# Kernel tuning notes

Hardware: AMD Instinct MI355X
Metric: run time of the kernel (lower is better)

The kernel has to match this reference:

```python
import jax, jax.numpy as jnp
import numpy as np

B, S, D, H, DK, DV, SEG = 2, 4096, 1024, 8, 128, 128, 512
NSEG = S // SEG


def setup_inputs() -> dict:
    key = jax.random.key(0)
    k0, k1, k2, k3, k4, k5 = jax.random.split(key, 6)
    return {
        "x": jax.random.normal(k0, (B, S, D), jnp.float32),
        "Wk": jax.random.normal(k1, (H, D, DK), jnp.float32) / np.float32(np.sqrt(D)),
        "Wv": jax.random.normal(k2, (H, D, DV), jnp.float32) / np.float32(np.sqrt(D)),
        "Wq": jax.random.normal(k3, (H, D, DK), jnp.float32) / np.float32(np.sqrt(D)),
        "Wout": jax.random.normal(k4, (H * DV, D), jnp.float32) / np.float32(np.sqrt(H * DV)),
        "betas": jax.random.normal(k5, (1, H, 1, DV), jnp.float32),
    }


def reference(x, Wk, Wv, Wq, Wout, betas):
    # Per-head projections: (B,H,S,dk/dv)
    k_full = jnp.einsum('bsd,hdk->bhsk', x, Wk)
    v_full = jnp.einsum('bsd,hdk->bhsk', x, Wv)
    q_full = jnp.einsum('bsd,hdk->bhsk', x, Wq)

    def to_segs(t):  # (B,H,S,E) -> (NSEG,B,H,SEG,E)
        return t.reshape(B, H, NSEG, SEG, t.shape[-1]).transpose(2, 0, 1, 3, 4)

    segs = (to_segs(k_full), to_segs(v_full), to_segs(q_full))

    mem0 = jnp.zeros((B, H, DK, DV), x.dtype)           # compressive memory
    z0 = jnp.full((B, H, DK, 1), 1.0 / DK, x.dtype)     # normalizer
    causal_mask = jnp.tril(jnp.ones((SEG, SEG), bool))
    gate = jax.nn.sigmoid(betas)                        # (1,H,1,DV)
    scale = jnp.asarray(1.0 / np.sqrt(DK), x.dtype)

    def step(carry, seg):
        mem, z = carry
        k, v, q = seg                                   # (B,H,SEG,dk/dv)
        sigma_q = jax.nn.elu(q) + 1.0
        # segment-local causal softmax attention
        scores = jnp.einsum('bhik,bhjk->bhij', q, k) * scale
        scores = jnp.where(causal_mask, scores, -jnp.inf)
        att_dot = jax.nn.softmax(scores, axis=-1) @ v
        # linear-attention read from memory
        att_mem = (sigma_q @ mem) / (sigma_q @ z)
        # delta-rule memory update
        sigma_k = jax.nn.elu(k) + 1.0
        mem = mem + jnp.einsum('bhsk,bhsv->bhkv', sigma_k, v - (sigma_k @ mem) / (sigma_k @ z))
        z = z + jnp.sum(sigma_k, axis=-2, keepdims=True).swapaxes(-1, -2)
        # gated mix of memory and local attention
        att = gate * att_mem + (1.0 - gate) * att_dot   # (B,H,SEG,DV)
        att = att.transpose(0, 2, 1, 3).reshape(B, SEG, H * DV)
        return (mem, z), att @ Wout                     # (B,SEG,D)

    _, outs = jax.lax.scan(step, (mem0, z0), segs)      # (NSEG,B,SEG,D)
    return outs.transpose(1, 0, 2, 3).reshape(B, S, D)
```

## Files before the change

kernel.cpp:

```cpp
#include <hip/hip_runtime.h>

#define B_  2
#define S_  4096
#define D_  1024
#define H_  8
#define DK_ 128
#define DV_ 128
#define SEG_ 512
#define NSEG_ 8
#define BH_ 16
#define M_ 8192

typedef __attribute__((ext_vector_type(8))) short bf16x8;
typedef __attribute__((ext_vector_type(4))) float f32x4;

__device__ __forceinline__ float elu1(float x) { return x > 0.f ? x + 1.f : __expf(x); }
__device__ __forceinline__ float sigmoidf(float x) { return 1.f / (1.f + __expf(-x)); }

__device__ __forceinline__ unsigned short f2b(float f) {
    union { float f; unsigned int u; } x; x.f = f;
    unsigned int r = x.u + 0x7fffu + ((x.u >> 16) & 1u);
    return (unsigned short)(r >> 16);
}
__device__ __forceinline__ float b2f(unsigned short u) {
    union { unsigned int u; float f; } x; x.u = ((unsigned int)u) << 16; return x.f;
}

__device__ __forceinline__ void gl2lds16(const void* g, void* l) {
    __builtin_amdgcn_global_load_lds(
        (const __attribute__((address_space(1))) void*)g,
        (__attribute__((address_space(3))) void*)l, 16, 0, 0);
}

__global__ __launch_bounds__(256) void conv_bf16(
    const float* __restrict__ src, unsigned short* __restrict__ dst)
{
    int i = (blockIdx.x * 256 + threadIdx.x) * 4;
    float4 v = *(const float4*)(src + i);
    ushort4 o;
    o.x = f2b(v.x); o.y = f2b(v.y); o.z = f2b(v.z); o.w = f2b(v.w);
    *(ushort4*)(dst + i) = o;
}

__global__ __launch_bounds__(256) void transpose_conv(
    const float* __restrict__ src, unsigned short* __restrict__ dst, int R, int C)
{
    __shared__ float tile[32][33];
    const size_t moff = (size_t)blockIdx.z * R * C;
    src += moff; dst += moff;
    const int c0 = blockIdx.x * 32, r0 = blockIdx.y * 32;
    const int tx = threadIdx.x & 31, ty = threadIdx.x >> 5;
    #pragma unroll
    for (int i = 0; i < 32; i += 8)
        tile[ty + i][tx] = src[(size_t)(r0 + ty + i) * C + c0 + tx];
    __syncthreads();
    #pragma unroll
    for (int i = 0; i < 32; i += 8)
        dst[(size_t)(c0 + ty + i) * R + r0 + tx] = f2b(tile[tx][ty + i]);
}

__global__ __launch_bounds__(256) void colsum_k(
    const unsigned short* __restrict__ Kbb, float* __restrict__ colsum)
{
    __shared__ float red[32][128];
    const int t = threadIdx.x;
    const int bh = blockIdx.x >> 3, seg = blockIdx.x & 7;
    const unsigned short* Kp = Kbb + ((size_t)bh * 4096 + seg * 512) * 128;
    const int rbase = t >> 3, c0 = (t & 7) * 16;
    float part[16] = {};
    for (int chunk = 0; chunk < 16; ++chunk) {
        const unsigned short* p = Kp + (size_t)(chunk * 32 + rbase) * 128 + c0;
        bf16x8 a = *(const bf16x8*)p;
        bf16x8 b = *(const bf16x8*)(p + 8);
        #pragma unroll
        for (int j = 0; j < 8; ++j) {
            part[j]     += elu1(b2f((unsigned short)a[j]));
            part[j + 8] += elu1(b2f((unsigned short)b[j]));
        }
    }
    #pragma unroll
    for (int j = 0; j < 16; ++j) red[rbase][c0 + j] = part[j];
    __syncthreads();
    if (t < 128) {
        float s = 0.f;
        #pragma unroll
        for (int r = 0; r < 32; ++r) s += red[r][t];
        colsum[(size_t)blockIdx.x * 128 + t] = s;
    }
}

__global__ __launch_bounds__(256) void den_z(
    const unsigned short* __restrict__ Kbb, const float* __restrict__ colsum,
    float* __restrict__ den, float* __restrict__ zseg)
{
    __shared__ float zs[128];
    const int t = threadIdx.x;
    const int bh = blockIdx.x >> 3, seg = blockIdx.x & 7;
    if (t < 128) {
        float z = 1.f / 128.f;
        for (int j = 0; j < seg; ++j) z += colsum[(size_t)(bh * 8 + j) * 128 + t];
        zs[t] = z;
        zseg[(size_t)blockIdx.x * 128 + t] = z;
    }
    __syncthreads();
    #pragma unroll
    for (int rr = 0; rr < 2; ++rr) {
        int s = t + rr * 256;
        const unsigned short* kp = Kbb + ((size_t)bh * 4096 + seg * 512 + s) * 128;
        float d = 0.f;
        #pragma unroll 4
        for (int f = 0; f < 16; ++f) {
            bf16x8 a = *(const bf16x8*)(kp + f * 8);
            #pragma unroll
            for (int j = 0; j < 8; ++j)
                d += elu1(b2f((unsigned short)a[j])) * zs[f * 8 + j];
        }
        den[(size_t)bh * 4096 + seg * 512 + s] = d;
    }
}

__global__ __launch_bounds__(256) void sigma_kT2(
    const unsigned short* __restrict__ Kbb, const float* __restrict__ den,
    unsigned short* __restrict__ SkT, unsigned short* __restrict__ SkTs)
{
    __shared__ float tile[32][33];
    __shared__ float rden[32];
    const int bh = blockIdx.z;
    const int s0 = blockIdx.x * 32, dk0 = blockIdx.y * 32;
    const int tx = threadIdx.x & 31, ty = threadIdx.x >> 5;
    if (threadIdx.x < 32) rden[threadIdx.x] = 1.f / den[(size_t)bh * 4096 + s0 + threadIdx.x];
    #pragma unroll
    for (int i = 0; i < 32; i += 8)
        tile[ty + i][tx] = elu1(b2f(Kbb[((size_t)bh * 4096 + s0 + ty + i) * 128 + dk0 + tx]));
    __syncthreads();
    #pragma unroll
    for (int i = 0; i < 32; i += 8) {
        float v = tile[tx][ty + i];
        size_t o = ((size_t)bh * 128 + dk0 + ty + i) * 4096 + s0 + tx;
        SkT[o]  = f2b(v);
        SkTs[o] = f2b(v * rden[tx]);
    }
}

__device__ __forceinline__ void mfma_gemm_128(
    const unsigned short* __restrict__ A, int lda,
    const unsigned short* __restrict__ Bt, int ldb, int K,
    unsigned short* As, unsigned short* Bs, f32x4 acc[4][4])
{
    const int tid = threadIdx.x;
    const int wave = tid >> 6, lane = tid & 63;
    const int r4 = lane >> 2;
    const int c4s = (((lane & 3) ^ ((lane >> 2) & 3)) * 8);
    const int lrow = lane & 15, lquad = lane >> 4;
    const int sl8 = (lquad ^ (lrow & 3)) * 8;
    const int wm = (wave >> 1) * 64, wn = (wave & 1) * 64;
    const int ar0 = wave * 32, ar1 = wave * 32 + 16;
    const int T = K >> 5;

    auto STAGE = [&](int t, int bufidx) {
        unsigned short* Ab = As + bufidx * 4096;
        unsigned short* Bb = Bs + bufidx * 4096;
        const int kk = t * 32;
        gl2lds16(A  + (size_t)(ar0 + r4) * lda + kk + c4s, Ab + ar0 * 32);
        gl2lds16(A  + (size_t)(ar1 + r4) * lda + kk + c4s, Ab + ar1 * 32);
        gl2lds16(Bt + (size_t)(ar0 + r4) * ldb + kk + c4s, Bb + ar0 * 32);
        gl2lds16(Bt + (size_t)(ar1 + r4) * ldb + kk + c4s, Bb + ar1 * 32);
    };

    STAGE(0, 0);
    STAGE(1, 1);
    int cur = 0;
    for (int t = 0; t < T; ++t) {
        if (t + 2 < T) {
            int nb = cur + 2; if (nb >= 3) nb -= 3;
            STAGE(t + 2, nb);
            asm volatile("s_waitcnt vmcnt(8)" ::: "memory");
        } else if (t + 1 < T) {
            asm volatile("s_waitcnt vmcnt(4)" ::: "memory");
        } else {
            asm volatile("s_waitcnt vmcnt(0)" ::: "memory");
        }
        __builtin_amdgcn_s_barrier();
        __builtin_amdgcn_sched_barrier(0);
        const unsigned short* Ac = As + cur * 4096;
        const unsigned short* Bc = Bs + cur * 4096;
        bf16x8 af[4], bfr[4];
        #pragma unroll
        for (int i = 0; i < 4; ++i)
            af[i] = *(const bf16x8*)(Ac + (wm + i * 16 + lrow) * 32 + sl8);
        #pragma unroll
        for (int j = 0; j < 4; ++j)
            bfr[j] = *(const bf16x8*)(Bc + (wn + j * 16 + lrow) * 32 + sl8);
        #pragma unroll
        for (int i = 0; i < 4; ++i)
            #pragma unroll
            for (int j = 0; j < 4; ++j)
                acc[i][j] = __builtin_amdgcn_mfma_f32_16x16x32_bf16(af[i], bfr[j], acc[i][j], 0, 0, 0);
        __builtin_amdgcn_s_barrier();
        __builtin_amdgcn_sched_barrier(0);
        cur += 1; if (cur >= 3) cur -= 3;
    }
}

__global__ __launch_bounds__(256) void gemm_qkv_mfma(
    const unsigned short* __restrict__ xb, const unsigned short* __restrict__ Wtb,
    unsigned short* __restrict__ Qbb, unsigned short* __restrict__ Kbb,
    unsigned short* __restrict__ Vtb)
{
    __shared__ unsigned short As[3 * 128 * 32];
    __shared__ unsigned short Bs[3 * 128 * 32];
    const int m0 = blockIdx.x * 128;
    const int panel = blockIdx.y;
    const int which = panel >> 3, h = panel & 7;
    f32x4 acc[4][4] = {};
    mfma_gemm_128(xb + (size_t)m0 * 1024, 1024,
                  Wtb + (size_t)panel * 128 * 1024, 1024, 1024, As, Bs, acc);
    const int tid = threadIdx.x, wave = tid >> 6, lane = tid & 63;
    const int lrow = lane & 15, lquad = lane >> 4;
    const int wm = (wave >> 1) * 64, wn = (wave & 1) * 64;
    #pragma unroll
    for (int i = 0; i < 4; ++i)
        #pragma unroll
        for (int r = 0; r < 4; ++r) {
            int m = m0 + wm + i * 16 + lquad * 4 + r;
            int bb = m >> 12, s = m & 4095;
            int bh = bb * 8 + h;
            size_t rowbase = ((size_t)bh * 4096 + s) * 128;
            #pragma unroll
            for (int j = 0; j < 4; ++j) {
                int col = wn + j * 16 + lrow;
                unsigned short v = f2b(acc[i][j][r]);
                if (which == 0) Kbb[rowbase + col] = v;
                else if (which == 1)
                    Vtb[(((size_t)bh * 8 + (s >> 9)) * 128 + col) * 512 + (s & 511)] = v;
                else Qbb[rowbase + col] = v;
            }
        }
}

__global__ __launch_bounds__(256) void gemm_out_mfma(
    const unsigned short* __restrict__ A, const unsigned short* __restrict__ Bt,
    float* __restrict__ C)
{
    __shared__ unsigned short As[3 * 128 * 32];
    __shared__ unsigned short Bs[3 * 128 * 32];
    const int m0 = blockIdx.x * 128, n0 = blockIdx.y * 128;
    f32x4 acc[4][4] = {};
    mfma_gemm_128(A + (size_t)m0 * 1024, 1024,
                  Bt + (size_t)n0 * 1024, 1024, 1024, As, Bs, acc);
    const int tid = threadIdx.x, wave = tid >> 6, lane = tid & 63;
    const int lrow = lane & 15, lquad = lane >> 4;
    const int wm = (wave >> 1) * 64, wn = (wave & 1) * 64;
    #pragma unroll
    for (int i = 0; i < 4; ++i)
        #pragma unroll
        for (int r = 0; r < 4; ++r) {
            int m = m0 + wm + i * 16 + lquad * 4 + r;
            #pragma unroll
            for (int j = 0; j < 4; ++j)
                C[(size_t)m * 1024 + n0 + wn + j * 16 + lrow] = acc[i][j][r];
        }
}

__global__ __launch_bounds__(256) void ac_gemm(
    const unsigned short* __restrict__ SkT, const unsigned short* __restrict__ SkTs,
    const unsigned short* __restrict__ Vtb,
    unsigned short* __restrict__ Emat, float* __restrict__ Cmat)
{
    __shared__ unsigned short As[2 * 128 * 32];
    __shared__ unsigned short Bs1[2 * 128 * 32];
    __shared__ unsigned short Bs2[2 * 128 * 32];
    const int bh = blockIdx.x >> 3, seg = blockIdx.x & 7;
    const unsigned short* Ap  = SkT  + (size_t)bh * 128 * 4096 + seg * 512;
    const unsigned short* B1p = SkTs + (size_t)bh * 128 * 4096 + seg * 512;
    const unsigned short* B2p = Vtb  + (size_t)blockIdx.x * 128 * 512;
    const int tid = threadIdx.x;
    const int wave = tid >> 6, lane = tid & 63;
    const int r4 = lane >> 2;
    const int c4s = (((lane & 3) ^ ((lane >> 2) & 3)) * 8);
    const int lrow = lane & 15, lquad = lane >> 4;
    const int sl8 = (lquad ^ (lrow & 3)) * 8;
    const int wm = (wave >> 1) * 64, wn = (wave & 1) * 64;
    const int ar0 = wave * 32, ar1 = wave * 32 + 16;
    f32x4 e[4][4] = {}, c[4][4] = {};
    gl2lds16(Ap  + (size_t)(ar0 + r4) * 4096 + c4s, As  + ar0 * 32);
    gl2lds16(Ap  + (size_t)(ar1 + r4) * 4096 + c4s, As  + ar1 * 32);
    gl2lds16(B1p + (size_t)(ar0 + r4) * 4096 + c4s, Bs1 + ar0 * 32);
    gl2lds16(B1p + (size_t)(ar1 + r4) * 4096 + c4s, Bs1 + ar1 * 32);
    gl2lds16(B2p + (size_t)(ar0 + r4) * 512  + c4s, Bs2 + ar0 * 32);
    gl2lds16(B2p + (size_t)(ar1 + r4) * 512  + c4s, Bs2 + ar1 * 32);
    __syncthreads();
    int cur = 0;
    for (int k0 = 0; k0 < 512; k0 += 32) {
        if (k0 + 32 < 512) {
            unsigned short* An  = As  + (cur ^ 1) * 4096;
            unsigned short* B1n = Bs1 + (cur ^ 1) * 4096;
            unsigned short* B2n = Bs2 + (cur ^ 1) * 4096;
            const int kn = k0 + 32;
            gl2lds16(Ap  + (size_t)(ar0 + r4) * 4096 + kn + c4s, An  + ar0 * 32);
            gl2lds16(Ap  + (size_t)(ar1 + r4) * 4096 + kn + c4s, An  + ar1 * 32);
            gl2lds16(B1p + (size_t)(ar0 + r4) * 4096 + kn + c4s, B1n + ar0 * 32);
            gl2lds16(B1p + (size_t)(ar1 + r4) * 4096 + kn + c4s, B1n + ar1 * 32);
            gl2lds16(B2p + (size_t)(ar0 + r4) * 512  + kn + c4s, B2n + ar0 * 32);
            gl2lds16(B2p + (size_t)(ar1 + r4) * 512  + kn + c4s, B2n + ar1 * 32);
        }
        const unsigned short* Ac  = As  + cur * 4096;
        const unsigned short* B1c = Bs1 + cur * 4096;
        const unsigned short* B2c = Bs2 + cur * 4096;
        bf16x8 af[4], b1[4], b2[4];
        #pragma unroll
        for (int i = 0; i < 4; ++i)
            af[i] = *(const bf16x8*)(Ac + (wm + i * 16 + lrow) * 32 + sl8);
        #pragma unroll
        for (int j = 0; j < 4; ++j) {
            b1[j] = *(const bf16x8*)(B1c + (wn + j * 16 + lrow) * 32 + sl8);
            b2[j] = *(const bf16x8*)(B2c + (wn + j * 16 + lrow) * 32 + sl8);
        }
        #pragma unroll
        for (int i = 0; i < 4; ++i)
            #pragma unroll
            for (int j = 0; j < 4; ++j) {
                e[i][j] = __builtin_amdgcn_mfma_f32_16x16x32_bf16(af[i], b1[j], e[i][j], 0, 0, 0);
                c[i][j] = __builtin_amdgcn_mfma_f32_16x16x32_bf16(af[i], b2[j], c[i][j], 0, 0, 0);
            }
        __syncthreads();
        cur ^= 1;
    }
    #pragma unroll
    for (int i = 0; i < 4; ++i)
        #pragma unroll
        for (int r = 0; r < 4; ++r) {
            int m = wm + i * 16 + lquad * 4 + r;
            #pragma unroll
            for (int j = 0; j < 4; ++j) {
                int nn = wn + j * 16 + lrow;
                size_t o = (size_t)blockIdx.x * 16384 + (size_t)m * 128 + nn;
                Emat[o] = f2b(-e[i][j][r]);
                Cmat[o] = c[i][j][r];
            }
        }
}

__global__ __launch_bounds__(512) void scan_step(
    const unsigned short* __restrict__ Emat, const float* __restrict__ Cmat,
    unsigned short* __restrict__ Memb)
{
    __shared__ unsigned short msh[128][136];
    const int t = threadIdx.x;
    const int wv = t >> 6, lane = t & 63;
    const int n16 = lane & 15, quad = lane >> 4;
    const int bh = blockIdx.x;
    f32x4 macc[8] = {};
    for (int seg = 0; seg < 8; ++seg) {
        unsigned short* gm = Memb + ((size_t)(bh * 8 + seg)) * 16384;
        #pragma unroll
        for (int vt = 0; vt < 8; ++vt) {
            ushort4 o;
            o.x = f2b(macc[vt][0]); o.y = f2b(macc[vt][1]);
            o.z = f2b(macc[vt][2]); o.w = f2b(macc[vt][3]);
            *(ushort4*)&msh[vt * 16 + n16][wv * 16 + quad * 4] = o;
            *(ushort4*)(gm + (size_t)(vt * 16 + n16) * 128 + wv * 16 + quad * 4) = o;
        }
        if (seg == 7) break;
        __syncthreads();
        const unsigned short* Ep = Emat + ((size_t)(bh * 8 + seg)) * 16384
                                 + (size_t)(wv * 16 + n16) * 128;
        bf16x8 ea[4];
        #pragma unroll
        for (int kf = 0; kf < 4; ++kf)
            ea[kf] = *(const bf16x8*)(Ep + kf * 32 + quad * 8);
        const float* Cp = Cmat + ((size_t)(bh * 8 + seg)) * 16384
                        + (size_t)(wv * 16 + quad * 4) * 128;
        #pragma unroll
        for (int vt = 0; vt < 8; ++vt)
            #pragma unroll
            for (int r = 0; r < 4; ++r)
                macc[vt][r] += Cp[(size_t)r * 128 + vt * 16 + n16];
        #pragma unroll
        for (int vt = 0; vt < 8; ++vt)
            #pragma unroll
            for (int kf = 0; kf < 4; ++kf) {
                bf16x8 bfr = *(const bf16x8*)&msh[vt * 16 + n16][kf * 32 + quad * 8];
                macc[vt] = __builtin_amdgcn_mfma_f32_16x16x32_bf16(ea[kf], bfr, macc[vt], 0, 0, 0);
            }
        __syncthreads();
    }
}

__global__ __launch_bounds__(256) void attn_out(
    const unsigned short* __restrict__ Qbb, const unsigned short* __restrict__ Kbb,
    const unsigned short* __restrict__ Vtb, const unsigned short* __restrict__ Memb,
    const float* __restrict__ zseg, const float* __restrict__ betas,
    unsigned short* __restrict__ Attb)
{
    __shared__ unsigned short Pl[4][32][72];
    const int tid = threadIdx.x, wave = tid >> 6, lane = tid & 63;
    const int n = lane & 15, quad = lane >> 4;
    const int bh = blockIdx.x >> 3, seg = blockIdx.x & 7;
    const int a = blockIdx.y;
    const int qt = (wave < 2) ? a : 7 - a;
    const int sp = (wave & 1) * 2;
    const int b = bh >> 3, h = bh & 7;
    const float scale2 = 0.12751744979f;
    const float FSH2 = 23.083120654f;

    const unsigned short* Qp = Qbb + ((size_t)bh * 4096 + seg * 512 + qt * 64 + sp * 16) * 128;
    const unsigned short* Kp = Kbb + ((size_t)bh * 4096 + seg * 512) * 128;
    const unsigned short* Vp = Vtb + ((size_t)bh * 8 + seg) * 128 * 512;

    bf16x8 aQ[2][4];
    #pragma unroll
    for (int s = 0; s < 2; ++s)
        #pragma unroll
        for (int kc = 0; kc < 4; ++kc)
            aQ[s][kc] = *(const bf16x8*)(Qp + (size_t)(s * 16 + n) * 128 + kc * 32 + quad * 8);

    f32x4 O[2][8] = {};
    float lpart[2][4] = {};

    for (int jt = 0; jt <= qt; ++jt) {
        f32x4 Sf[2][4] = {};
        #pragma unroll
        for (int kc = 0; kc < 4; ++kc) {
            bf16x8 bK[4];
            #pragma unroll
            for (int ns = 0; ns < 4; ++ns)
                bK[ns] = *(const bf16x8*)(Kp + (size_t)(jt * 64 + ns * 16 + n) * 128 + kc * 32 + quad * 8);
            #pragma unroll
            for (int ns = 0; ns < 4; ++ns) {
                Sf[0][ns] = __builtin_amdgcn_mfma_f32_16x16x32_bf16(aQ[0][kc], bK[ns], Sf[0][ns], 0, 0, 0);
                Sf[1][ns] = __builtin_amdgcn_mfma_f32_16x16x32_bf16(aQ[1][kc], bK[ns], Sf[1][ns], 0, 0, 0);
            }
        }
        const bool diag = (jt == qt);
        #pragma unroll
        for (int s = 0; s < 2; ++s)
            #pragma unroll
            for (int reg = 0; reg < 4; ++reg) {
                #pragma unroll
                for (int ns = 0; ns < 4; ++ns) {
                    float sv = Sf[s][ns][reg] * scale2 - FSH2;
                    if (diag) {
                        int grow = qt * 64 + (sp + s) * 16 + quad * 4 + reg;
                        int gcol = jt * 64 + ns * 16 + n;
                        if (gcol > grow) sv = -1e30f;
                    }
                    float p = exp2f(sv);
                    lpart[s][reg] += p;
                    Pl[wave][s * 16 + quad * 4 + reg][ns * 16 + n] = f2b(p);
                }
            }
        bf16x8 aP[2][2];
        #pragma unroll
        for (int s = 0; s < 2; ++s) {
            aP[s][0] = *(const bf16x8*)&Pl[wave][s * 16 + n][quad * 8];
            aP[s][1] = *(const bf16x8*)&Pl[wave][s * 16 + n][32 + quad * 8];
        }
        #pragma unroll
        for (int dvs = 0; dvs < 8; ++dvs) {
            bf16x8 bV0 = *(const bf16x8*)(Vp + (size_t)(dvs * 16 + n) * 512 + jt * 64 + quad * 8);
            bf16x8 bV1 = *(const bf16x8*)(Vp + (size_t)(dvs * 16 + n) * 512 + jt * 64 + 32 + quad * 8);
            O[0][dvs] = __builtin_amdgcn_mfma_f32_16x16x32_bf16(aP[0][0], bV0, O[0][dvs], 0, 0, 0);
            O[0][dvs] = __builtin_amdgcn_mfma_f32_16x16x32_bf16(aP[0][1], bV1, O[0][dvs], 0, 0, 0);
            O[1][dvs] = __builtin_amdgcn_mfma_f32_16x16x32_bf16(aP[1][0], bV0, O[1][dvs], 0, 0, 0);
            O[1][dvs] = __builtin_amdgcn_mfma_f32_16x16x32_bf16(aP[1][1], bV1, O[1][dvs], 0, 0, 0);
        }
    }
    const float* zp = zseg + (size_t)(bh * 8 + seg) * 128;
    const unsigned short* Mp = Memb + (size_t)(bh * 8 + seg) * 16384;
    #pragma unroll
    for (int s = 0; s < 2; ++s) {
        float l_i[4];
        #pragma unroll
        for (int r = 0; r < 4; ++r) {
            float rs = lpart[s][r];
            rs += __shfl_xor(rs, 1);
            rs += __shfl_xor(rs, 2);
            rs += __shfl_xor(rs, 4);
            rs += __shfl_xor(rs, 8);
            l_i[r] = rs;
        }
        float den = 0.f;
        bf16x8 aS[4];
        #pragma unroll
        for (int kc = 0; kc < 4; ++kc) {
            float4 z0 = *(const float4*)(zp + kc * 32 + quad * 8);
            float4 z1 = *(const float4*)(zp + kc * 32 + quad * 8 + 4);
            float zv[8] = {z0.x, z0.y, z0.z, z0.w, z1.x, z1.y, z1.z, z1.w};
            bf16x8 aa;
            #pragma unroll
            for (int j = 0; j < 8; ++j) {
                float sv = elu1(b2f((unsigned short)aQ[s][kc][j]));
                den += sv * zv[j];
                aa[j] = (short)f2b(sv);
            }
            aS[kc] = aa;
        }
        den += __shfl_xor(den, 16);
        den += __shfl_xor(den, 32);
        f32x4 Om[8] = {};
        #pragma unroll
        for (int dvs = 0; dvs < 8; ++dvs)
            #pragma unroll
            for (int kc = 0; kc < 4; ++kc) {
                bf16x8 bm = *(const bf16x8*)(Mp + (size_t)(dvs * 16 + n) * 128 + kc * 32 + quad * 8);
                Om[dvs] = __builtin_amdgcn_mfma_f32_16x16x32_bf16(aS[kc], bm, Om[dvs], 0, 0, 0);
            }
        float irm[4], inv[4];
        #pragma unroll
        for (int r = 0; r < 4; ++r) {
            irm[r] = 1.f / __shfl(den, quad * 4 + r);
            inv[r] = 1.f / l_i[r];
        }
        #pragma unroll
        for (int dvs = 0; dvs < 8; ++dvs) {
            int dv = dvs * 16 + n;
            float g = sigmoidf(betas[h * 128 + dv]);
            #pragma unroll
            for (int r = 0; r < 4; ++r) {
                int srow = seg * 512 + qt * 64 + (sp + s) * 16 + quad * 4 + r;
                float val = g * Om[dvs][r] * irm[r] + (1.f - g) * O[s][dvs][r] * inv[r];
                Attb[((size_t)b * 4096 + srow) * 1024 + h * 128 + dv] = f2b(val);
            }
        }
    }
}

extern "C" void kernel_launch(void* const* d_in, const int* in_sizes, int n_in,
                              void* d_out, int out_size, void* d_ws, size_t ws_size,
                              hipStream_t stream) {
    const float* x     = (const float*)d_in[0];
    const float* Wk    = (const float*)d_in[1];
    const float* Wv    = (const float*)d_in[2];
    const float* Wq    = (const float*)d_in[3];
    const float* Wout  = (const float*)d_in[4];
    const float* betas = (const float*)d_in[5];
    float* out = (float*)d_out;

    unsigned short* Qbb  = (unsigned short*)d_ws;
    unsigned short* Kbb  = Qbb + 8388608;
    unsigned short* Vtb  = Kbb + 8388608;
    unsigned short* SkT  = Vtb + 8388608;
    unsigned short* SkTs = SkT + 8388608;
    unsigned short* Emat = SkTs + 8388608;
    unsigned short* Memb = Emat + 2097152;
    float* Cmat   = (float*)(Memb + 2097152);
    float* colsum = Cmat + 2097152;
    float* zseg   = colsum + 16384;
    float* den    = zseg + 16384;
    unsigned short* xb    = SkT;
    unsigned short* Wtb   = SkTs;
    unsigned short* Attb  = SkT;
    unsigned short* Woutb = SkTs;

    conv_bf16<<<8192, 256, 0, stream>>>(x, xb);
    transpose_conv<<<dim3(4, 32, 8), 256, 0, stream>>>(Wk, Wtb,               1024, 128);
    transpose_conv<<<dim3(4, 32, 8), 256, 0, stream>>>(Wv, Wtb +  8 * 131072, 1024, 128);
    transpose_conv<<<dim3(4, 32, 8), 256, 0, stream>>>(Wq, Wtb + 16 * 131072, 1024, 128);
    gemm_qkv_mfma<<<dim3(64, 24), 256, 0, stream>>>(xb, Wtb, Qbb, Kbb, Vtb);
    colsum_k<<<128, 256, 0, stream>>>(Kbb, colsum);
    den_z<<<128, 256, 0, stream>>>(Kbb, colsum, den, zseg);
    sigma_kT2<<<dim3(128, 4, 16), 256, 0, stream>>>(Kbb, den, SkT, SkTs);
    ac_gemm<<<128, 256, 0, stream>>>(SkT, SkTs, Vtb, Emat, Cmat);
    scan_step<<<16, 512, 0, stream>>>(Emat, Cmat, Memb);
    attn_out<<<dim3(128, 4), 256, 0, stream>>>(Qbb, Kbb, Vtb, Memb, zseg, betas, Attb);
    transpose_conv<<<dim3(32, 32, 1), 256, 0, stream>>>(Wout, Woutb, 1024, 1024);
    gemm_out_mfma<<<dim3(64, 8), 256, 0, stream>>>(Attb, Woutb, out);
}
```

Measured before the change: 362.2 us.

## Merge weight transposes, vectorize V-transpose stores, triple-buffer ac_gemm loads

The three Wk/Wv/Wq transpose-convert launches become a single launch that picks its source by blockIdx.z, cutting launch overhead. In the QKV GEMM epilogue, the transposed V stores are grouped into 4-wide ushort4 writes instead of scattered 2-byte stores. The ac_gemm K loop goes from double to triple buffering, with explicit vmcnt waits and raw barriers so loads run two stages ahead. The extra LDS may lower occupancy, and the hand-written waitcnt counts depend on how many memory instructions each stage issues.

```diff
diff --git a/kernel.cpp b/kernel.cpp
--- a/kernel.cpp
+++ b/kernel.cpp
@@ -57,6 +57,27 @@
     #pragma unroll
     for (int i = 0; i < 32; i += 8)
         dst[(size_t)(c0 + ty + i) * R + r0 + tx] = f2b(tile[tx][ty + i]);
+}
+
+__global__ __launch_bounds__(256) void transpose_conv3(
+    const float* __restrict__ Wk, const float* __restrict__ Wv,
+    const float* __restrict__ Wq, unsigned short* __restrict__ dst)
+{
+    __shared__ float tile[32][33];
+    const int z = blockIdx.z;
+    const int w = z >> 3;
+    const float* src = (w == 0) ? Wk : (w == 1) ? Wv : Wq;
+    src += (size_t)(z & 7) * 131072;
+    dst += (size_t)z * 131072;
+    const int c0 = blockIdx.x * 32, r0 = blockIdx.y * 32;
+    const int tx = threadIdx.x & 31, ty = threadIdx.x >> 5;
+    #pragma unroll
+    for (int i = 0; i < 32; i += 8)
+        tile[ty + i][tx] = src[(size_t)(r0 + ty + i) * 128 + c0 + tx];
+    __syncthreads();
+    #pragma unroll
+    for (int i = 0; i < 32; i += 8)
+        dst[(size_t)(c0 + ty + i) * 1024 + r0 + tx] = f2b(tile[tx][ty + i]);
 }
 
 __global__ __launch_bounds__(256) void colsum_k(
@@ -218,24 +239,37 @@
     const int tid = threadIdx.x, wave = tid >> 6, lane = tid & 63;
     const int lrow = lane & 15, lquad = lane >> 4;
     const int wm = (wave >> 1) * 64, wn = (wave & 1) * 64;
-    #pragma unroll
-    for (int i = 0; i < 4; ++i)
-        #pragma unroll
-        for (int r = 0; r < 4; ++r) {
-            int m = m0 + wm + i * 16 + lquad * 4 + r;
-            int bb = m >> 12, s = m & 4095;
+    if (which == 1) {
+        #pragma unroll
+        for (int i = 0; i < 4; ++i) {
+            int mb = m0 + wm + i * 16 + lquad * 4;
+            int bb = mb >> 12, sb = mb & 4095;
             int bh = bb * 8 + h;
-            size_t rowbase = ((size_t)bh * 4096 + s) * 128;
+            size_t vbase = ((size_t)bh * 8 + (sb >> 9)) * 128;
             #pragma unroll
             for (int j = 0; j < 4; ++j) {
                 int col = wn + j * 16 + lrow;
-                unsigned short v = f2b(acc[i][j][r]);
-                if (which == 0) Kbb[rowbase + col] = v;
-                else if (which == 1)
-                    Vtb[(((size_t)bh * 8 + (s >> 9)) * 128 + col) * 512 + (s & 511)] = v;
-                else Qbb[rowbase + col] = v;
-            }
-        }
+                ushort4 o;
+                o.x = f2b(acc[i][j][0]); o.y = f2b(acc[i][j][1]);
+                o.z = f2b(acc[i][j][2]); o.w = f2b(acc[i][j][3]);
+                *(ushort4*)(Vtb + ((vbase + col) * 512 + (sb & 511))) = o;
+            }
+        }
+    } else {
+        unsigned short* Dst = (which == 0) ? Kbb : Qbb;
+        #pragma unroll
+        for (int i = 0; i < 4; ++i)
+            #pragma unroll
+            for (int r = 0; r < 4; ++r) {
+                int m = m0 + wm + i * 16 + lquad * 4 + r;
+                int bb = m >> 12, s = m & 4095;
+                int bh = bb * 8 + h;
+                size_t rowbase = ((size_t)bh * 4096 + s) * 128;
+                #pragma unroll
+                for (int j = 0; j < 4; ++j)
+                    Dst[rowbase + wn + j * 16 + lrow] = f2b(acc[i][j][r]);
+            }
+    }
 }
 
 __global__ __launch_bounds__(256) void gemm_out_mfma(
@@ -267,9 +301,9 @@
     const unsigned short* __restrict__ Vtb,
     unsigned short* __restrict__ Emat, float* __restrict__ Cmat)
 {
-    __shared__ unsigned short As[2 * 128 * 32];
-    __shared__ unsigned short Bs1[2 * 128 * 32];
-    __shared__ unsigned short Bs2[2 * 128 * 32];
+    __shared__ unsigned short As [3 * 128 * 32];
+    __shared__ unsigned short Bs1[3 * 128 * 32];
+    __shared__ unsigned short Bs2[3 * 128 * 32];
     const int bh = blockIdx.x >> 3, seg = blockIdx.x & 7;
     const unsigned short* Ap  = SkT  + (size_t)bh * 128 * 4096 + seg * 512;
     const unsigned short* B1p = SkTs + (size_t)bh * 128 * 4096 + seg * 512;
@@ -283,27 +317,35 @@
     const int wm = (wave >> 1) * 64, wn = (wave & 1) * 64;
     const int ar0 = wave * 32, ar1 = wave * 32 + 16;
     f32x4 e[4][4] = {}, c[4][4] = {};
-    gl2lds16(Ap  + (size_t)(ar0 + r4) * 4096 + c4s, As  + ar0 * 32);
-    gl2lds16(Ap  + (size_t)(ar1 + r4) * 4096 + c4s, As  + ar1 * 32);
-    gl2lds16(B1p + (size_t)(ar0 + r4) * 4096 + c4s, Bs1 + ar0 * 32);
-    gl2lds16(B1p + (size_t)(ar1 + r4) * 4096 + c4s, Bs1 + ar1 * 32);
-    gl2lds16(B2p + (size_t)(ar0 + r4) * 512  + c4s, Bs2 + ar0 * 32);
-    gl2lds16(B2p + (size_t)(ar1 + r4) * 512  + c4s, Bs2 + ar1 * 32);
-    __syncthreads();
+
+    auto STAGE = [&](int t, int bufidx) {
+        unsigned short* Ab  = As  + bufidx * 4096;
+        unsigned short* B1b = Bs1 + bufidx * 4096;
+        unsigned short* B2b = Bs2 + bufidx * 4096;
+        const int kk = t * 32;
+        gl2lds16(Ap  + (size_t)(ar0 + r4) * 4096 + kk + c4s, Ab  + ar0 * 32);
+        gl2lds16(Ap  + (size_t)(ar1 + r4) * 4096 + kk + c4s, Ab  + ar1 * 32);
+        gl2lds16(B1p + (size_t)(ar0 + r4) * 4096 + kk + c4s, B1b + ar0 * 32);
+        gl2lds16(B1p + (size_t)(ar1 + r4) * 4096 + kk + c4s, B1b + ar1 * 32);
+        gl2lds16(B2p + (size_t)(ar0 + r4) * 512  + kk + c4s, B2b + ar0 * 32);
+        gl2lds16(B2p + (size_t)(ar1 + r4) * 512  + kk + c4s, B2b + ar1 * 32);
+    };
+
+    STAGE(0, 0);
+    STAGE(1, 1);
     int cur = 0;
-    for (int k0 = 0; k0 < 512; k0 += 32) {
-        if (k0 + 32 < 512) {
-            unsigned short* An  = As  + (cur ^ 1) * 4096;
-            unsigned short* B1n = Bs1 + (cur ^ 1) * 4096;
-            unsigned short* B2n = Bs2 + (cur ^ 1) * 4096;
-            const int kn = k0 + 32;
-            gl2lds16(Ap  + (size_t)(ar0 + r4) * 4096 + kn + c4s, An  + ar0 * 32);
-            gl2lds16(Ap  + (size_t)(ar1 + r4) * 4096 + kn + c4s, An  + ar1 * 32);
-            gl2lds16(B1p + (size_t)(ar0 + r4) * 4096 + kn + c4s, B1n + ar0 * 32);
-            gl2lds16(B1p + (size_t)(ar1 + r4) * 4096 + kn + c4s, B1n + ar1 * 32);
-            gl2lds16(B2p + (size_t)(ar0 + r4) * 512  + kn + c4s, B2n + ar0 * 32);
-            gl2lds16(B2p + (size_t)(ar1 + r4) * 512  + kn + c4s, B2n + ar1 * 32);
-        }
+    for (int t = 0; t < 16; ++t) {
+        if (t + 2 < 16) {
+            int nb = cur + 2; if (nb >= 3) nb -= 3;
+            STAGE(t + 2, nb);
+            asm volatile("s_waitcnt vmcnt(12)" ::: "memory");
+        } else if (t + 1 < 16) {
+            asm volatile("s_waitcnt vmcnt(6)" ::: "memory");
+        } else {
+            asm volatile("s_waitcnt vmcnt(0)" ::: "memory");
+        }
+        __builtin_amdgcn_s_barrier();
+        __builtin_amdgcn_sched_barrier(0);
         const unsigned short* Ac  = As  + cur * 4096;
         const unsigned short* B1c = Bs1 + cur * 4096;
         const unsigned short* B2c = Bs2 + cur * 4096;
@@ -323,8 +365,9 @@
                 e[i][j] = __builtin_amdgcn_mfma_f32_16x16x32_bf16(af[i], b1[j], e[i][j], 0, 0, 0);
                 c[i][j] = __builtin_amdgcn_mfma_f32_16x16x32_bf16(af[i], b2[j], c[i][j], 0, 0, 0);
             }
-        __syncthreads();
-        cur ^= 1;
+        __builtin_amdgcn_s_barrier();
+        __builtin_amdgcn_sched_barrier(0);
+        cur += 1; if (cur >= 3) cur -= 3;
     }
     #pragma unroll
     for (int i = 0; i < 4; ++i)
@@ -554,9 +597,7 @@
     unsigned short* Woutb = SkTs;
 
     conv_bf16<<<8192, 256, 0, stream>>>(x, xb);
-    transpose_conv<<<dim3(4, 32, 8), 256, 0, stream>>>(Wk, Wtb,               1024, 128);
-    transpose_conv<<<dim3(4, 32, 8), 256, 0, stream>>>(Wv, Wtb +  8 * 131072, 1024, 128);
-    transpose_conv<<<dim3(4, 32, 8), 256, 0, stream>>>(Wq, Wtb + 16 * 131072, 1024, 128);
+    transpose_conv3<<<dim3(4, 32, 24), 256, 0, stream>>>(Wk, Wv, Wq, Wtb);
     gemm_qkv_mfma<<<dim3(64, 24), 256, 0, stream>>>(xb, Wtb, Qbb, Kbb, Vtb);
     colsum_k<<<128, 256, 0, stream>>>(Kbb, colsum);
     den_z<<<128, 256, 0, stream>>>(Kbb, colsum, den, zseg);
```

New measurement: 358.9 us. Within noise of the previous version (-0.9%).
